# Performance work log

Measured on AMD Instinct MI355X. Metric: run time of the kernel, lower is better.

## Reference

```python
import jax, jax.numpy as jnp
import numpy as np

SEQ_LEN = 96      # args.seq_len (in_feats)
H_FEATS = 100
OUT_FEATS = 128
HEADS = 4
K = 64            # args.input_size = nodes per graph
B = 256           # number of graphs (batch_size)
N = K * B
DEG = 8
E = N * DEG
OUT_SIZE = 24     # args.output_size
NEG_SLOPE = 0.2   # PyG GATConv default


def setup_inputs() -> dict:
    key = jax.random.key(0)
    ks = jax.random.split(key, 20)
    s = 0.05
    x = jax.random.normal(ks[0], (N, SEQ_LEN), jnp.float32)
    # intra-graph random edges (dst repeated, src within same graph)
    dst = jnp.repeat(jnp.arange(N, dtype=jnp.int32), DEG)
    src = (dst // K) * K + jax.random.randint(ks[1], (E,), 0, K, dtype=jnp.int32)
    edge_index = jnp.stack([src, dst])
    batch = jnp.repeat(jnp.arange(B, dtype=jnp.int32), K)
    y = jax.random.normal(ks[2], (N, OUT_SIZE), jnp.float32)
    # GATConv 1: in=96 -> heads=4, ch=100
    W1 = jax.random.normal(ks[3], (SEQ_LEN, HEADS * H_FEATS), jnp.float32) * s
    as1 = jax.random.normal(ks[4], (HEADS, H_FEATS), jnp.float32) * s
    ad1 = jax.random.normal(ks[5], (HEADS, H_FEATS), jnp.float32) * s
    b1 = jnp.zeros((H_FEATS,), jnp.float32)
    # GATConv 2: in=100 -> heads=4, ch=128
    W2 = jax.random.normal(ks[6], (H_FEATS, HEADS * OUT_FEATS), jnp.float32) * s
    as2 = jax.random.normal(ks[7], (HEADS, OUT_FEATS), jnp.float32) * s
    ad2 = jax.random.normal(ks[8], (HEADS, OUT_FEATS), jnp.float32) * s
    b2 = jnp.zeros((OUT_FEATS,), jnp.float32)
    # per-node-index MLPs (batched over K)
    fw1 = jax.random.normal(ks[9], (K, OUT_FEATS, 64), jnp.float32) * s
    fb1 = jnp.zeros((K, 64), jnp.float32)
    fw2 = jax.random.normal(ks[10], (K, 64, OUT_SIZE), jnp.float32) * s
    fb2 = jnp.zeros((K, OUT_SIZE), jnp.float32)
    return dict(x=x, edge_index=edge_index, batch=batch, y=y,
                W1=W1, as1=as1, ad1=ad1, b1=b1,
                W2=W2, as2=as2, ad2=ad2, b2=b2,
                fw1=fw1, fb1=fb1, fw2=fw2, fb2=fb2)


def gat_conv(x, src, dst, W, a_src, a_dst, bias):
    # PyG GATConv (concat=False): linear -> per-edge attention -> softmax over
    # incoming edges of each dst -> weighted sum -> mean over heads + bias.
    n = x.shape[0]
    xl = (x @ W).reshape(n, HEADS, -1)                      # [N,H,C]
    al_src = jnp.sum(xl * a_src, axis=-1)                   # [N,H]
    al_dst = jnp.sum(xl * a_dst, axis=-1)                   # [N,H]
    alpha = jax.nn.leaky_relu(al_src[src] + al_dst[dst], NEG_SLOPE)  # [E,H]
    m = jax.ops.segment_max(alpha, dst, num_segments=n)
    ea = jnp.exp(alpha - m[dst])
    denom = jax.ops.segment_sum(ea, dst, num_segments=n)
    w = ea / (denom[dst] + 1e-16)                           # [E,H]
    msg = xl[src] * w[:, :, None]                           # [E,H,C]
    out = jax.ops.segment_sum(msg, dst, num_segments=n)     # [N,H,C]
    return out.mean(axis=1) + bias                          # concat=False


def reference(x, edge_index, batch, y, W1, as1, ad1, b1, W2, as2, ad2, b2, fw1, fb1, fw2, fb2):
    n = x.shape[0]
    src, dst = edge_index[0], edge_index[1]
    loop = jnp.arange(n, dtype=src.dtype)                   # GATConv adds self-loops
    src = jnp.concatenate([src, loop])
    dst = jnp.concatenate([dst, loop])
    h = jax.nn.elu(gat_conv(x, src, dst, W1, as1, ad1, b1))
    h = gat_conv(h, src, dst, W2, as2, ad2, b2)             # [N,128]
    # batch is sorted with K nodes per graph -> stacking == static reshape
    xg = h.reshape(B, K, OUT_FEATS).transpose(1, 0, 2)      # [K,B,128]
    hid = jax.nn.relu(jnp.einsum('kbi,kih->kbh', xg, fw1) + fb1[:, None, :])
    pred = jnp.einsum('kbh,kho->kbo', hid, fw2) + fb2[:, None, :]  # [K,B,out]
    yg = y.reshape(B, K, OUT_SIZE)                          # [B,K,out]
    return pred, yg
```

## Files before the change

kernel.cpp:

```cpp
#include <hip/hip_runtime.h>
#include <hip/hip_bf16.h>
#include <math.h>


#define N_NODES 16384
#define B_GRAPHS 256
#define K_NODES 64
#define DEG 8
#define NHEADS 4
#define C1 100
#define C2 128
#define IN_F 96
#define HID 64
#define OUT_SZ 24
#define PRED_ELEMS (K_NODES * B_GRAPHS * OUT_SZ)

#define W1T_ROWS 448
#define W1T_K    96
#define W2T_ROWS 512
#define W2T_K    128

using bf16 = __hip_bfloat16;
typedef __attribute__((ext_vector_type(8))) short          frag_ab;
typedef __attribute__((ext_vector_type(4))) float          frag_cd;
typedef unsigned short us8 __attribute__((ext_vector_type(8)));
typedef unsigned short us4 __attribute__((ext_vector_type(4)));

__device__ __forceinline__ float us2f(unsigned short u) {
  return __bfloat162float(__ushort_as_bfloat16(u));
}
__device__ __forceinline__ short f2bf_s(float f) {
  return __builtin_bit_cast(short, __float2bfloat16(f));
}

__global__ __launch_bounds__(256)
void pack_w(const float* __restrict__ W1, const float* __restrict__ W2,
            bf16* __restrict__ W1t, bf16* __restrict__ W2t) {
  int idx = blockIdx.x * 256 + threadIdx.x;
  if (idx < W1T_ROWS * W1T_K) {
    int c = idx / W1T_K, k = idx - c * W1T_K;
    W1t[idx] = __float2bfloat16((c < 400) ? W1[(size_t)k * 400 + c] : 0.f);
  } else {
    int i2 = idx - W1T_ROWS * W1T_K;
    if (i2 < W2T_ROWS * W2T_K) {
      int c = i2 >> 7, k = i2 & 127;
      W2t[i2] = __float2bfloat16((k < 100) ? W2[(size_t)k * 512 + c] : 0.f);
    }
  }
}

template<int KDIM, int KP, int C, bool ELU, typename AT>
__global__ __launch_bounds__(256)
void gat_layer(const AT* __restrict__ A, const bf16* __restrict__ Wt,
               const int* __restrict__ esrc,
               const float* __restrict__ a_src, const float* __restrict__ a_dst,
               const float* __restrict__ bias, bf16* __restrict__ out) {
  constexpr int C4  = NHEADS * C;
  constexpr int NCH = (C4 + 63) / 64;
  constexpr int C4P = NCH * 64;
  constexpr int NT  = (C + 15) / 16;
  constexpr int LDA = KP + 8;
  constexpr int LDT = 72;
  constexpr int LDP = 72;

  __shared__ __align__(16) short          As[64 * LDA];
  __shared__ __align__(16) unsigned short xs[C4P * LDT];
  __shared__ __align__(16) short          Ps[NHEADS * 64 * LDP];
  __shared__ float avs[C4], avd[C4], bia[C];
  __shared__ int   edg[K_NODES * DEG];
  __shared__ float als[64 * 5], ald[64 * 5];

  const int g = blockIdx.x;
  const int t = threadIdx.x;

  if constexpr (sizeof(AT) == 4) {
    constexpr int QR = KDIM / 4;
    for (int idx = t; idx < 64 * QR; idx += 256) {
      int m = idx / QR, q = idx - m * QR;
      const float4 v = *(const float4*)((const float*)A +
                                        ((size_t)(g * 64 + m) * KDIM + q * 4));
      short* d = &As[m * LDA + q * 4];
      d[0] = f2bf_s(v.x); d[1] = f2bf_s(v.y); d[2] = f2bf_s(v.z); d[3] = f2bf_s(v.w);
    }
  } else {
    constexpr int PR = KDIM / 2;
    for (int idx = t; idx < 64 * PR; idx += 256) {
      int m = idx / PR, p = idx - m * PR;
      const ushort2 v = *(const ushort2*)((const unsigned short*)A +
                                          ((size_t)(g * 64 + m) * KDIM + p * 2));
      As[m * LDA + p * 2]     = (short)v.x;
      As[m * LDA + p * 2 + 1] = (short)v.y;
    }
  }
  if constexpr (KP > KDIM) {
    constexpr int TR = KP - KDIM;
    for (int idx = t; idx < 64 * TR; idx += 256) {
      int m = idx / TR, kk = idx - m * TR;
      As[m * LDA + KDIM + kk] = 0;
    }
  }
  for (int idx = t; idx < C4; idx += 256) { avs[idx] = a_src[idx]; avd[idx] = a_dst[idx]; }
  for (int idx = t; idx < C;  idx += 256) bia[idx] = bias[idx];
  for (int idx = t; idx < K_NODES * DEG; idx += 256)
    edg[idx] = esrc[g * K_NODES * DEG + idx] & (K_NODES - 1);
  for (int idx = t; idx < NHEADS * 64 * LDP / 8; idx += 256)
    *(us8*)&Ps[idx * 8] = (us8)0;
  __syncthreads();

  const int wv = t >> 6;
  const int l  = t & 63;
  const int lm = l & 15;
  const int lk = (l >> 4) * 8;
  const int rq = (l >> 4) * 4;

  for (int ch = wv; ch < NCH; ch += 4) {
    const int n0 = ch * 64;
    frag_cd acc[4][4] = {};
#pragma unroll
    for (int ks = 0; ks < KP; ks += 32) {
      frag_ab b[4];
#pragma unroll
      for (int nt = 0; nt < 4; ++nt)
        b[nt] = *(const frag_ab*)((const short*)Wt +
                                  (size_t)(n0 + nt * 16 + lm) * KP + ks + lk);
#pragma unroll
      for (int mt = 0; mt < 4; ++mt) {
        frag_ab a = *(const frag_ab*)&As[(mt * 16 + lm) * LDA + ks + lk];
#pragma unroll
        for (int nt = 0; nt < 4; ++nt)
          acc[mt][nt] = __builtin_amdgcn_mfma_f32_16x16x32_bf16(a, b[nt],
                                                                acc[mt][nt], 0, 0, 0);
      }
    }
#pragma unroll
    for (int mt = 0; mt < 4; ++mt) {
#pragma unroll
      for (int nt = 0; nt < 4; ++nt) {
        const int c4 = n0 + nt * 16 + lm;
        us4 o;
#pragma unroll
        for (int r = 0; r < 4; ++r) o[r] = (unsigned short)f2bf_s(acc[mt][nt][r]);
        *(us4*)&xs[c4 * LDT + mt * 16 + rq] = o;
      }
    }
  }
  __syncthreads();

  {
    const int h = wv, n = l;
    float ss = 0.f, sd = 0.f;
#pragma unroll 4
    for (int c = 0; c < C; ++c) {
      const float v = us2f(xs[(h * C + c) * LDT + n]);
      ss += v * avs[h * C + c];
      sd += v * avd[h * C + c];
    }
    als[n * 5 + h] = ss;
    ald[n * 5 + h] = sd;
  }
  __syncthreads();

  {
    const int n = t >> 2, h = t & 3;
    const float ad = ald[n * 5 + h];
    int   sv[9];
    float a[9];
#pragma unroll
    for (int j = 0; j < 8; ++j) sv[j] = edg[n * DEG + j];
    sv[8] = n;
#pragma unroll
    for (int j = 0; j < 9; ++j) {
      float v = als[sv[j] * 5 + h] + ad;
      a[j] = (v >= 0.f) ? v : 0.2f * v;
    }
    float m = -1e30f;
#pragma unroll
    for (int j = 0; j < 9; ++j) m = fmaxf(m, a[j]);
    float s = 0.f;
#pragma unroll
    for (int j = 0; j < 9; ++j) { a[j] = __expf(a[j] - m); s += a[j]; }
    const float inv = 1.f / (s + 1e-16f);
    short* prow = &Ps[(h * 64 + n) * LDP];
#pragma unroll
    for (int j = 0; j < 9; ++j) {
      float tw = a[j];
#pragma unroll
      for (int i = 0; i < 9; ++i)
        if (i != j && sv[i] == sv[j]) tw += a[i];
      prow[sv[j]] = f2bf_s(tw * inv);
    }
  }
  __syncthreads();

  {
    const int mw = wv * 16;
    frag_cd acc[NT] = {};
#pragma unroll
    for (int h = 0; h < NHEADS; ++h) {
#pragma unroll
      for (int ks = 0; ks < 64; ks += 32) {
        frag_ab a = *(const frag_ab*)&Ps[(h * 64 + mw + lm) * LDP + ks + lk];
#pragma unroll
        for (int nt = 0; nt < NT; ++nt) {
          frag_ab b = *(const frag_ab*)&xs[(h * C + nt * 16 + lm) * LDT + ks + lk];
          acc[nt] = __builtin_amdgcn_mfma_f32_16x16x32_bf16(a, b, acc[nt], 0, 0, 0);
        }
      }
    }
    unsigned short* outp = (unsigned short*)out + (size_t)(g * 64) * C;
#pragma unroll
    for (int nt = 0; nt < NT; ++nt) {
      const int c = nt * 16 + lm;
      if (c < C) {
        const float bc = bia[c];
#pragma unroll
        for (int r = 0; r < 4; ++r) {
          float vv = acc[nt][r] * 0.25f + bc;
          if (ELU) vv = (vv > 0.f) ? vv : (__expf(vv) - 1.f);
          outp[(size_t)(mw + rq + r) * C + c] = (unsigned short)f2bf_s(vv);
        }
      }
    }
  }
}

__global__ __launch_bounds__(256)
void mlp_mfma(const bf16* __restrict__ h2,
              const float* __restrict__ fw1, const float* __restrict__ fb1,
              const float* __restrict__ fw2, const float* __restrict__ fb2,
              float* __restrict__ pred) {
  constexpr int LDA = C2 + 8;
  constexpr int LDH = HID + 8;
  __shared__ __align__(16) short As[64 * LDA];
  __shared__ __align__(16) short B1[HID * LDA];
  __shared__ __align__(16) short Hs[64 * LDH];
  __shared__ __align__(16) short B2[32 * LDH];
  __shared__ float b1s[HID];
  __shared__ float b2s[32];

  const int k  = blockIdx.x & 63;
  const int ms = blockIdx.x >> 6;
  const int t  = threadIdx.x;

  for (int idx = t; idx < 64 * 16; idx += 256) {
    int r = idx >> 4, o = idx & 15;
    const us8 v = *(const us8*)((const unsigned short*)h2 +
        ((size_t)((ms * 64 + r) * K_NODES + k) * C2) + o * 8);
    *(us8*)&As[r * LDA + o * 8] = v;
  }
  for (int idx = t; idx < C2 * HID; idx += 256) {
    int kk = idx >> 6, n = idx & 63;
    B1[n * LDA + kk] = f2bf_s(fw1[(size_t)k * C2 * HID + kk * HID + n]);
  }
  for (int idx = t; idx < HID * 32; idx += 256) {
    int kk = idx >> 5, n = idx & 31;
    float v = (n < OUT_SZ) ? fw2[(size_t)k * HID * OUT_SZ + kk * OUT_SZ + n] : 0.f;
    B2[n * LDH + kk] = f2bf_s(v);
  }
  if (t < HID) b1s[t] = fb1[k * HID + t];
  if (t < 32)  b2s[t] = (t < OUT_SZ) ? fb2[k * OUT_SZ + t] : 0.f;
  __syncthreads();

  const int wv = t >> 6;
  const int l  = t & 63;
  const int lm = l & 15;
  const int lk = (l >> 4) * 8;
  const int rq = (l >> 4) * 4;

  frag_cd acc[4] = {};
#pragma unroll
  for (int ks = 0; ks < C2; ks += 32) {
    frag_ab a = *(const frag_ab*)&As[(wv * 16 + lm) * LDA + ks + lk];
#pragma unroll
    for (int nt = 0; nt < 4; ++nt) {
      frag_ab b = *(const frag_ab*)&B1[(nt * 16 + lm) * LDA + ks + lk];
      acc[nt] = __builtin_amdgcn_mfma_f32_16x16x32_bf16(a, b, acc[nt], 0, 0, 0);
    }
  }
#pragma unroll
  for (int nt = 0; nt < 4; ++nt) {
    const int j  = nt * 16 + lm;
    const float bj = b1s[j];
#pragma unroll
    for (int r = 0; r < 4; ++r) {
      const int m = wv * 16 + rq + r;
      Hs[m * LDH + j] = f2bf_s(fmaxf(acc[nt][r] + bj, 0.f));
    }
  }
  __syncthreads();

  frag_cd acc2[2] = {};
#pragma unroll
  for (int ks = 0; ks < HID; ks += 32) {
    frag_ab a = *(const frag_ab*)&Hs[(wv * 16 + lm) * LDH + ks + lk];
#pragma unroll
    for (int nt = 0; nt < 2; ++nt) {
      frag_ab b = *(const frag_ab*)&B2[(nt * 16 + lm) * LDH + ks + lk];
      acc2[nt] = __builtin_amdgcn_mfma_f32_16x16x32_bf16(a, b, acc2[nt], 0, 0, 0);
    }
  }
#pragma unroll
  for (int nt = 0; nt < 2; ++nt) {
    const int q = nt * 16 + lm;
    if (q < OUT_SZ) {
      const float bq = b2s[q];
#pragma unroll
      for (int r = 0; r < 4; ++r) {
        const int m = wv * 16 + rq + r;
        pred[((size_t)k * B_GRAPHS + ms * 64 + m) * OUT_SZ + q] = acc2[nt][r] + bq;
      }
    }
  }
}

__global__ __launch_bounds__(256)
void yg_kernel(const float* __restrict__ y, float* __restrict__ dst) {
  int i = (blockIdx.x * 256 + threadIdx.x) * 4;
  float4 v = *(const float4*)(y + i);
  v.x = __bfloat162float(__float2bfloat16(v.x));
  v.y = __bfloat162float(__float2bfloat16(v.y));
  v.z = __bfloat162float(__float2bfloat16(v.z));
  v.w = __bfloat162float(__float2bfloat16(v.w));
  *(float4*)(dst + i) = v;
}

extern "C" void kernel_launch(void* const* d_in, const int* in_sizes, int n_in,
                              void* d_out, int out_size, void* d_ws, size_t ws_size,
                              hipStream_t stream) {
  const float* x   = (const float*)d_in[0];
  const int*   ei  = (const int*)d_in[1];
  const float* y   = (const float*)d_in[3];
  const float* W1  = (const float*)d_in[4];
  const float* as1 = (const float*)d_in[5];
  const float* ad1 = (const float*)d_in[6];
  const float* b1  = (const float*)d_in[7];
  const float* W2  = (const float*)d_in[8];
  const float* as2 = (const float*)d_in[9];
  const float* ad2 = (const float*)d_in[10];
  const float* b2  = (const float*)d_in[11];
  const float* fw1 = (const float*)d_in[12];
  const float* fb1 = (const float*)d_in[13];
  const float* fw2 = (const float*)d_in[14];
  const float* fb2 = (const float*)d_in[15];

  bf16* h1  = (bf16*)d_ws;
  bf16* h2  = h1 + (size_t)N_NODES * C1;
  bf16* W1t = h2 + (size_t)N_NODES * C2;
  bf16* W2t = W1t + W1T_ROWS * W1T_K;

  float* out = (float*)d_out;

  const int pack_elems = W1T_ROWS * W1T_K + W2T_ROWS * W2T_K;
  pack_w<<<(pack_elems + 255) / 256, 256, 0, stream>>>(W1, W2, W1t, W2t);

  gat_layer<IN_F, IN_F, C1, true, float>
      <<<B_GRAPHS, 256, 0, stream>>>(x, W1t, ei, as1, ad1, b1, h1);
  gat_layer<C1, 128, C2, false, unsigned short>
      <<<B_GRAPHS, 256, 0, stream>>>((const unsigned short*)h1, W2t, ei,
                                     as2, ad2, b2, h2);

  mlp_mfma<<<K_NODES * 4, 256, 0, stream>>>(h2, fw1, fb1, fw2, fb2, out);

  yg_kernel<<<PRED_ELEMS / 4 / 256, 256, 0, stream>>>(y, out + PRED_ELEMS);
}
```

Measured before the change: 127.4 us.

## Fuse both GAT layers into one per-graph kernel and merge prep kernels

Result: faster. 118.6 us (-6.9%).

```diff
diff --git a/kernel.cpp b/kernel.cpp
--- a/kernel.cpp
+++ b/kernel.cpp
@@ -33,99 +33,97 @@
   return __builtin_bit_cast(short, __float2bfloat16(f));
 }
 
+#define P1N (W1T_ROWS * W1T_K)
+#define P2N (W2T_ROWS * W2T_K)
+#define YG4 (PRED_ELEMS / 4)
+
 __global__ __launch_bounds__(256)
-void pack_w(const float* __restrict__ W1, const float* __restrict__ W2,
-            bf16* __restrict__ W1t, bf16* __restrict__ W2t) {
+void prep(const float* __restrict__ W1, const float* __restrict__ W2,
+          const float* __restrict__ y,
+          bf16* __restrict__ W1t, bf16* __restrict__ W2t,
+          float* __restrict__ yg) {
   int idx = blockIdx.x * 256 + threadIdx.x;
-  if (idx < W1T_ROWS * W1T_K) {
+  if (idx < P1N) {
     int c = idx / W1T_K, k = idx - c * W1T_K;
     W1t[idx] = __float2bfloat16((c < 400) ? W1[(size_t)k * 400 + c] : 0.f);
+  } else if (idx < P1N + P2N) {
+    int i2 = idx - P1N;
+    int c = i2 >> 7, k = i2 & 127;
+    W2t[i2] = __float2bfloat16((k < 100) ? W2[(size_t)k * 512 + c] : 0.f);
   } else {
-    int i2 = idx - W1T_ROWS * W1T_K;
-    if (i2 < W2T_ROWS * W2T_K) {
-      int c = i2 >> 7, k = i2 & 127;
-      W2t[i2] = __float2bfloat16((k < 100) ? W2[(size_t)k * 512 + c] : 0.f);
-    }
-  }
-}
-
-template<int KDIM, int KP, int C, bool ELU, typename AT>
-__global__ __launch_bounds__(256)
-void gat_layer(const AT* __restrict__ A, const bf16* __restrict__ Wt,
+    int j = idx - P1N - P2N;
+    if (j < YG4) {
+      int i = j * 4;
+      float4 v = *(const float4*)(y + i);
+      v.x = __bfloat162float(__float2bfloat16(v.x));
+      v.y = __bfloat162float(__float2bfloat16(v.y));
+      v.z = __bfloat162float(__float2bfloat16(v.z));
+      v.w = __bfloat162float(__float2bfloat16(v.w));
+      *(float4*)(yg + i) = v;
+    }
+  }
+}
+
+__global__ __launch_bounds__(512)
+void gat_fused(const float* __restrict__ x,
+               const bf16* __restrict__ W1t, const bf16* __restrict__ W2t,
                const int* __restrict__ esrc,
-               const float* __restrict__ a_src, const float* __restrict__ a_dst,
-               const float* __restrict__ bias, bf16* __restrict__ out) {
-  constexpr int C4  = NHEADS * C;
-  constexpr int NCH = (C4 + 63) / 64;
-  constexpr int C4P = NCH * 64;
-  constexpr int NT  = (C + 15) / 16;
-  constexpr int LDA = KP + 8;
-  constexpr int LDT = 72;
-  constexpr int LDP = 72;
-
-  __shared__ __align__(16) short          As[64 * LDA];
-  __shared__ __align__(16) unsigned short xs[C4P * LDT];
-  __shared__ __align__(16) short          Ps[NHEADS * 64 * LDP];
-  __shared__ float avs[C4], avd[C4], bia[C];
+               const float* __restrict__ as1, const float* __restrict__ ad1,
+               const float* __restrict__ b1,
+               const float* __restrict__ as2, const float* __restrict__ ad2,
+               const float* __restrict__ b2,
+               bf16* __restrict__ h2out) {
+  constexpr int LDA1 = IN_F + 8;
+  constexpr int LDA2 = 136;
+  constexpr int LDT  = 72;
+
+  __shared__ __align__(16) short          As[64 * LDA2];
+  __shared__ __align__(16) unsigned short xs[512 * LDT];
+  __shared__ __align__(16) short          Ps[NHEADS * 64 * LDT];
+  __shared__ float avs1[400], avd1[400], avs2[512], avd2[512];
+  __shared__ float bia1[C1], bia2[C2];
   __shared__ int   edg[K_NODES * DEG];
   __shared__ float als[64 * 5], ald[64 * 5];
 
   const int g = blockIdx.x;
   const int t = threadIdx.x;
-
-  if constexpr (sizeof(AT) == 4) {
-    constexpr int QR = KDIM / 4;
-    for (int idx = t; idx < 64 * QR; idx += 256) {
-      int m = idx / QR, q = idx - m * QR;
-      const float4 v = *(const float4*)((const float*)A +
-                                        ((size_t)(g * 64 + m) * KDIM + q * 4));
-      short* d = &As[m * LDA + q * 4];
-      d[0] = f2bf_s(v.x); d[1] = f2bf_s(v.y); d[2] = f2bf_s(v.z); d[3] = f2bf_s(v.w);
-    }
-  } else {
-    constexpr int PR = KDIM / 2;
-    for (int idx = t; idx < 64 * PR; idx += 256) {
-      int m = idx / PR, p = idx - m * PR;
-      const ushort2 v = *(const ushort2*)((const unsigned short*)A +
-                                          ((size_t)(g * 64 + m) * KDIM + p * 2));
-      As[m * LDA + p * 2]     = (short)v.x;
-      As[m * LDA + p * 2 + 1] = (short)v.y;
-    }
-  }
-  if constexpr (KP > KDIM) {
-    constexpr int TR = KP - KDIM;
-    for (int idx = t; idx < 64 * TR; idx += 256) {
-      int m = idx / TR, kk = idx - m * TR;
-      As[m * LDA + KDIM + kk] = 0;
-    }
-  }
-  for (int idx = t; idx < C4; idx += 256) { avs[idx] = a_src[idx]; avd[idx] = a_dst[idx]; }
-  for (int idx = t; idx < C;  idx += 256) bia[idx] = bias[idx];
-  for (int idx = t; idx < K_NODES * DEG; idx += 256)
-    edg[idx] = esrc[g * K_NODES * DEG + idx] & (K_NODES - 1);
-  for (int idx = t; idx < NHEADS * 64 * LDP / 8; idx += 256)
-    *(us8*)&Ps[idx * 8] = (us8)0;
-  __syncthreads();
-
   const int wv = t >> 6;
   const int l  = t & 63;
   const int lm = l & 15;
   const int lk = (l >> 4) * 8;
   const int rq = (l >> 4) * 4;
 
-  for (int ch = wv; ch < NCH; ch += 4) {
-    const int n0 = ch * 64;
+  {
+    constexpr int QR = IN_F / 4;
+    for (int idx = t; idx < 64 * QR; idx += 512) {
+      int m = idx / QR, q = idx - m * QR;
+      const float4 v = *(const float4*)(x + ((size_t)(g * 64 + m) * IN_F + q * 4));
+      short* d = &As[m * LDA1 + q * 4];
+      d[0] = f2bf_s(v.x); d[1] = f2bf_s(v.y); d[2] = f2bf_s(v.z); d[3] = f2bf_s(v.w);
+    }
+  }
+  for (int idx = t; idx < 400; idx += 512) { avs1[idx] = as1[idx]; avd1[idx] = ad1[idx]; }
+  for (int idx = t; idx < 512; idx += 512) { avs2[idx] = as2[idx]; avd2[idx] = ad2[idx]; }
+  if (t < C1) bia1[t] = b1[t];
+  if (t < C2) bia2[t] = b2[t];
+  if (t < K_NODES * DEG) edg[t] = esrc[g * K_NODES * DEG + t] & (K_NODES - 1);
+  for (int idx = t; idx < NHEADS * 64 * LDT / 8; idx += 512)
+    *(us8*)&Ps[idx * 8] = (us8)0;
+  __syncthreads();
+
+  if (wv < 7) {
+    const int n0 = wv * 64;
     frag_cd acc[4][4] = {};
 #pragma unroll
-    for (int ks = 0; ks < KP; ks += 32) {
+    for (int ks = 0; ks < IN_F; ks += 32) {
       frag_ab b[4];
 #pragma unroll
       for (int nt = 0; nt < 4; ++nt)
-        b[nt] = *(const frag_ab*)((const short*)Wt +
-                                  (size_t)(n0 + nt * 16 + lm) * KP + ks + lk);
+        b[nt] = *(const frag_ab*)((const short*)W1t +
+                                  (size_t)(n0 + nt * 16 + lm) * W1T_K + ks + lk);
 #pragma unroll
       for (int mt = 0; mt < 4; ++mt) {
-        frag_ab a = *(const frag_ab*)&As[(mt * 16 + lm) * LDA + ks + lk];
+        frag_ab a = *(const frag_ab*)&As[(mt * 16 + lm) * LDA1 + ks + lk];
 #pragma unroll
         for (int nt = 0; nt < 4; ++nt)
           acc[mt][nt] = __builtin_amdgcn_mfma_f32_16x16x32_bf16(a, b[nt],
@@ -133,7 +131,7 @@
       }
     }
 #pragma unroll
-    for (int mt = 0; mt < 4; ++mt) {
+    for (int mt = 0; mt < 4; ++mt)
 #pragma unroll
       for (int nt = 0; nt < 4; ++nt) {
         const int c4 = n0 + nt * 16 + lm;
@@ -142,25 +140,24 @@
         for (int r = 0; r < 4; ++r) o[r] = (unsigned short)f2bf_s(acc[mt][nt][r]);
         *(us4*)&xs[c4 * LDT + mt * 16 + rq] = o;
       }
-    }
-  }
-  __syncthreads();
-
-  {
-    const int h = wv, n = l;
+  }
+  __syncthreads();
+
+  if (t < 256) {
+    const int n = t >> 2, h = t & 3;
     float ss = 0.f, sd = 0.f;
 #pragma unroll 4
-    for (int c = 0; c < C; ++c) {
-      const float v = us2f(xs[(h * C + c) * LDT + n]);
-      ss += v * avs[h * C + c];
-      sd += v * avd[h * C + c];
+    for (int c = 0; c < C1; ++c) {
+      const float v = us2f(xs[(h * C1 + c) * LDT + n]);
+      ss += v * avs1[h * C1 + c];
+      sd += v * avd1[h * C1 + c];
     }
     als[n * 5 + h] = ss;
     ald[n * 5 + h] = sd;
   }
   __syncthreads();
 
-  {
+  if (t < 256) {
     const int n = t >> 2, h = t & 3;
     const float ad = ald[n * 5 + h];
     int   sv[9];
@@ -180,7 +177,7 @@
 #pragma unroll
     for (int j = 0; j < 9; ++j) { a[j] = __expf(a[j] - m); s += a[j]; }
     const float inv = 1.f / (s + 1e-16f);
-    short* prow = &Ps[(h * 64 + n) * LDP];
+    short* prow = &Ps[(h * 64 + n) * LDT];
 #pragma unroll
     for (int j = 0; j < 9; ++j) {
       float tw = a[j];
@@ -189,36 +186,149 @@
         if (i != j && sv[i] == sv[j]) tw += a[i];
       prow[sv[j]] = f2bf_s(tw * inv);
     }
+  } else {
+    for (int i = t - 256; i < 64 * 28; i += 256) {
+      int m = i / 28, kk = 100 + (i - m * 28);
+      As[m * LDA2 + kk] = 0;
+    }
   }
   __syncthreads();
 
   {
-    const int mw = wv * 16;
-    frag_cd acc[NT] = {};
-#pragma unroll
-    for (int h = 0; h < NHEADS; ++h) {
+    const int mw = (wv & 3) * 16;
+    const int cg = wv >> 2;
+    const int ntb = cg * 4;
+    const int nte = (cg == 0) ? 4 : 7;
+    frag_cd acc[4] = {};
+#pragma unroll
+    for (int h = 0; h < NHEADS; ++h)
 #pragma unroll
       for (int ks = 0; ks < 64; ks += 32) {
-        frag_ab a = *(const frag_ab*)&Ps[(h * 64 + mw + lm) * LDP + ks + lk];
-#pragma unroll
-        for (int nt = 0; nt < NT; ++nt) {
-          frag_ab b = *(const frag_ab*)&xs[(h * C + nt * 16 + lm) * LDT + ks + lk];
+        frag_ab a = *(const frag_ab*)&Ps[(h * 64 + mw + lm) * LDT + ks + lk];
+        for (int nt = ntb; nt < nte; ++nt) {
+          frag_ab b = *(const frag_ab*)&xs[(h * C1 + nt * 16 + lm) * LDT + ks + lk];
+          acc[nt - ntb] = __builtin_amdgcn_mfma_f32_16x16x32_bf16(a, b,
+                                                                  acc[nt - ntb], 0, 0, 0);
+      }
+    }
+    for (int nt = ntb; nt < nte; ++nt) {
+      const int c = nt * 16 + lm;
+      if (c < C1) {
+        const float bc = bia1[c];
+#pragma unroll
+        for (int r = 0; r < 4; ++r) {
+          float vv = acc[nt - ntb][r] * 0.25f + bc;
+          vv = (vv > 0.f) ? vv : (__expf(vv) - 1.f);
+          As[(mw + rq + r) * LDA2 + c] = f2bf_s(vv);
+        }
+      }
+    }
+  }
+  __syncthreads();
+
+  {
+    const int n0 = wv * 64;
+    frag_cd acc[4][4] = {};
+#pragma unroll
+    for (int ks = 0; ks < 128; ks += 32) {
+      frag_ab b[4];
+#pragma unroll
+      for (int nt = 0; nt < 4; ++nt)
+        b[nt] = *(const frag_ab*)((const short*)W2t +
+                                  (size_t)(n0 + nt * 16 + lm) * W2T_K + ks + lk);
+#pragma unroll
+      for (int mt = 0; mt < 4; ++mt) {
+        frag_ab a = *(const frag_ab*)&As[(mt * 16 + lm) * LDA2 + ks + lk];
+#pragma unroll
+        for (int nt = 0; nt < 4; ++nt)
+          acc[mt][nt] = __builtin_amdgcn_mfma_f32_16x16x32_bf16(a, b[nt],
+                                                                acc[mt][nt], 0, 0, 0);
+      }
+    }
+#pragma unroll
+    for (int mt = 0; mt < 4; ++mt)
+#pragma unroll
+      for (int nt = 0; nt < 4; ++nt) {
+        const int c4 = n0 + nt * 16 + lm;
+        us4 o;
+#pragma unroll
+        for (int r = 0; r < 4; ++r) o[r] = (unsigned short)f2bf_s(acc[mt][nt][r]);
+        *(us4*)&xs[c4 * LDT + mt * 16 + rq] = o;
+      }
+  }
+  __syncthreads();
+
+  if (t < 256) {
+    const int n = t >> 2, h = t & 3;
+    float ss = 0.f, sd = 0.f;
+#pragma unroll 4
+    for (int c = 0; c < C2; ++c) {
+      const float v = us2f(xs[(h * C2 + c) * LDT + n]);
+      ss += v * avs2[h * C2 + c];
+      sd += v * avd2[h * C2 + c];
+    }
+    als[n * 5 + h] = ss;
+    ald[n * 5 + h] = sd;
+  }
+  __syncthreads();
+
+  if (t < 256) {
+    const int n = t >> 2, h = t & 3;
+    const float ad = ald[n * 5 + h];
+    int   sv[9];
+    float a[9];
+#pragma unroll
+    for (int j = 0; j < 8; ++j) sv[j] = edg[n * DEG + j];
+    sv[8] = n;
+#pragma unroll
+    for (int j = 0; j < 9; ++j) {
+      float v = als[sv[j] * 5 + h] + ad;
+      a[j] = (v >= 0.f) ? v : 0.2f * v;
+    }
+    float m = -1e30f;
+#pragma unroll
+    for (int j = 0; j < 9; ++j) m = fmaxf(m, a[j]);
+    float s = 0.f;
+#pragma unroll
+    for (int j = 0; j < 9; ++j) { a[j] = __expf(a[j] - m); s += a[j]; }
+    const float inv = 1.f / (s + 1e-16f);
+    short* prow = &Ps[(h * 64 + n) * LDT];
+#pragma unroll
+    for (int j = 0; j < 9; ++j) {
+      float tw = a[j];
+#pragma unroll
+      for (int i = 0; i < 9; ++i)
+        if (i != j && sv[i] == sv[j]) tw += a[i];
+      prow[sv[j]] = f2bf_s(tw * inv);
+    }
+  }
+  __syncthreads();
+
+  {
+    const int mw = (wv & 3) * 16;
+    const int cg = wv >> 2;
+    const int ntb = cg * 4;
+    frag_cd acc[4] = {};
+#pragma unroll
+    for (int h = 0; h < NHEADS; ++h)
+#pragma unroll
+      for (int ks = 0; ks < 64; ks += 32) {
+        frag_ab a = *(const frag_ab*)&Ps[(h * 64 + mw + lm) * LDT + ks + lk];
+#pragma unroll
+        for (int nt = 0; nt < 4; ++nt) {
+          frag_ab b = *(const frag_ab*)&xs[(h * C2 + (ntb + nt) * 16 + lm) * LDT + ks + lk];
           acc[nt] = __builtin_amdgcn_mfma_f32_16x16x32_bf16(a, b, acc[nt], 0, 0, 0);
         }
       }
-    }
-    unsigned short* outp = (unsigned short*)out + (size_t)(g * 64) * C;
-#pragma unroll
-    for (int nt = 0; nt < NT; ++nt) {
-      const int c = nt * 16 + lm;
-      if (c < C) {
-        const float bc = bia[c];
-#pragma unroll
-        for (int r = 0; r < 4; ++r) {
-          float vv = acc[nt][r] * 0.25f + bc;
-          if (ELU) vv = (vv > 0.f) ? vv : (__expf(vv) - 1.f);
-          outp[(size_t)(mw + rq + r) * C + c] = (unsigned short)f2bf_s(vv);
-        }
+    unsigned short* outp = (unsigned short*)h2out + (size_t)(g * 64) * C2;
+#pragma unroll
+    for (int nt = 0; nt < 4; ++nt) {
+      const int c = (ntb + nt) * 16 + lm;
+      const float bc = bia2[c];
+#pragma unroll
+      for (int r = 0; r < 4; ++r) {
+        float vv = acc[nt][r] * 0.25f + bc;
+        outp[(size_t)(mw + rq + r) * C2 + c] = (unsigned short)f2bf_s(vv);
       }
     }
   }
@@ -311,17 +421,6 @@
       }
     }
   }
-}
-
-__global__ __launch_bounds__(256)
-void yg_kernel(const float* __restrict__ y, float* __restrict__ dst) {
-  int i = (blockIdx.x * 256 + threadIdx.x) * 4;
-  float4 v = *(const float4*)(y + i);
-  v.x = __bfloat162float(__float2bfloat16(v.x));
-  v.y = __bfloat162float(__float2bfloat16(v.y));
-  v.z = __bfloat162float(__float2bfloat16(v.z));
-  v.w = __bfloat162float(__float2bfloat16(v.w));
-  *(float4*)(dst + i) = v;
 }
 
 extern "C" void kernel_launch(void* const* d_in, const int* in_sizes, int n_in,
@@ -343,23 +442,17 @@
   const float* fw2 = (const float*)d_in[14];
   const float* fb2 = (const float*)d_in[15];
 
-  bf16* h1  = (bf16*)d_ws;
-  bf16* h2  = h1 + (size_t)N_NODES * C1;
+  bf16* h2  = (bf16*)d_ws;
   bf16* W1t = h2 + (size_t)N_NODES * C2;
-  bf16* W2t = W1t + W1T_ROWS * W1T_K;
+  bf16* W2t = W1t + P1N;
 
   float* out = (float*)d_out;
 
-  const int pack_elems = W1T_ROWS * W1T_K + W2T_ROWS * W2T_K;
-  pack_w<<<(pack_elems + 255) / 256, 256, 0, stream>>>(W1, W2, W1t, W2t);
-
-  gat_layer<IN_F, IN_F, C1, true, float>
-      <<<B_GRAPHS, 256, 0, stream>>>(x, W1t, ei, as1, ad1, b1, h1);
-  gat_layer<C1, 128, C2, false, unsigned short>
-      <<<B_GRAPHS, 256, 0, stream>>>((const unsigned short*)h1, W2t, ei,
-                                     as2, ad2, b2, h2);
+  prep<<<(P1N + P2N + YG4 + 255) / 256, 256, 0, stream>>>(
+      W1, W2, y, W1t, W2t, out + PRED_ELEMS);
+
+  gat_fused<<<B_GRAPHS, 512, 0, stream>>>(x, W1t, W2t, ei,
+                                          as1, ad1, b1, as2, ad2, b2, h2);
 
   mlp_mfma<<<K_NODES * 4, 256, 0, stream>>>(h2, fw1, fb1, fw2, fb2, out);
-
-  yg_kernel<<<PRED_ELEMS / 4 / 256, 256, 0, stream>>>(y, out + PRED_ELEMS);
-}
+}
```
